# Kernel optimization log

Hardware: AMD Instinct MI355X
Metric: run time of the kernel (lower is better)

## Reference

```python
import jax, jax.numpy as jnp
import numpy as np

LN_EPS = 1e-6
L2_EPS = 1e-12


def _l2_normalize(v):
    # tf.nn.l2_normalize: v * rsqrt(max(sum(v^2), eps))
    ss = jnp.sum(v * v, axis=-1, keepdims=True)
    return v * jax.lax.rsqrt(jnp.maximum(ss, L2_EPS))


def setup_inputs() -> dict:
    key = jax.random.key(0)
    k1, k2, k3 = jax.random.split(key, 3)
    B, S, D, V = 4, 2048, 1024, 16384
    x = jax.random.normal(k1, (B, S, D), dtype=jnp.float32)
    dict_w = jax.random.normal(k2, (V, D), dtype=jnp.float32) * (2.0 / (V + D)) ** 0.5  # glorot_normal
    ln_gamma = jnp.ones((D,), dtype=jnp.float32)
    ln_beta = jnp.zeros((D,), dtype=jnp.float32)
    o_w = jax.random.normal(k3, (D, D), dtype=jnp.float32) * (2.0 / (D + D)) ** 0.5
    return {"x": x, "dict_w": dict_w, "ln_gamma": ln_gamma, "ln_beta": ln_beta, "o_w": o_w}


def reference(x, dict_w, ln_gamma, ln_beta, o_w):
    # cosine-sim codebook lookup
    q = _l2_normalize(x)                      # [B,S,D]
    k = _l2_normalize(dict_w)                 # [V,D]
    sim = jnp.einsum('bsd,vd->bsv', q, k)     # [B,S,V]
    word_idx = jnp.argmax(sim, axis=-1)       # [B,S] int
    word_sim = jnp.max(sim, axis=-1)          # [B,S]
    z = dict_w[word_idx]                      # gather codebook rows [B,S,D]
    # straight-through estimator
    e = jax.lax.stop_gradient(z - x) + x
    # layernorm (eps=1e-6)
    mu = jnp.mean(e, axis=-1, keepdims=True)
    var = jnp.mean(jnp.square(e - mu), axis=-1, keepdims=True)
    e_ln = (e - mu) * jax.lax.rsqrt(var + LN_EPS) * ln_gamma + ln_beta
    # output projection (no bias)
    out = jnp.einsum('bsd,de->bse', e_ln, o_w)
    return word_idx, word_sim, out
```

## Files before the change

kernel.cpp:

```cpp
#include <hip/hip_runtime.h>
#include <math.h>

#define D 1024
#define V 16384
#define NROWS 8192
#define NCAND 256
#define DELTA 0.15f

typedef __bf16 bf16_t;
typedef bf16_t bf16x8 __attribute__((ext_vector_type(8)));
typedef float f32x4 __attribute__((ext_vector_type(4)));
typedef int i32x4 __attribute__((ext_vector_type(4)));

__device__ __forceinline__ unsigned int sortable_key(float v) {
    unsigned int b = __float_as_uint(v);
    return (b & 0x80000000u) ? ~b : (b | 0x80000000u);
}
__device__ __forceinline__ float unkey(unsigned int key) {
    unsigned int b = (key & 0x80000000u) ? (key & 0x7FFFFFFFu) : ~key;
    return __uint_as_float(b);
}
__device__ __forceinline__ void split4(float4 v, uint2& hw, uint2& lw) {
    unsigned int u0 = __float_as_uint(v.x), u1 = __float_as_uint(v.y);
    unsigned int u2 = __float_as_uint(v.z), u3 = __float_as_uint(v.w);
    float l0 = v.x - __uint_as_float(u0 & 0xFFFF0000u);
    float l1 = v.y - __uint_as_float(u1 & 0xFFFF0000u);
    float l2 = v.z - __uint_as_float(u2 & 0xFFFF0000u);
    float l3 = v.w - __uint_as_float(u3 & 0xFFFF0000u);
    hw.x = (u0 >> 16) | (u1 & 0xFFFF0000u);
    hw.y = (u2 >> 16) | (u3 & 0xFFFF0000u);
    lw.x = (__float_as_uint(l0) >> 16) | (__float_as_uint(l1) & 0xFFFF0000u);
    lw.y = (__float_as_uint(l2) >> 16) | (__float_as_uint(l3) & 0xFFFF0000u);
}

__global__ __launch_bounds__(256) void prep_kernel(const float* __restrict__ W,
                                                   const float* __restrict__ X,
                                                   float* __restrict__ RK,
                                                   float* __restrict__ RQ,
                                                   float* __restrict__ SA,
                                                   float* __restrict__ SB,
                                                   float* __restrict__ RKS,
                                                   unsigned long long* __restrict__ packed,
                                                   unsigned int* __restrict__ count) {
    int tid = threadIdx.x;
    int row = blockIdx.x * 4 + (tid >> 6);
    int lane = tid & 63;
    const float* src = (row < V) ? (W + (size_t)row * D) : (X + (size_t)(row - V) * D);
    const float4* p = (const float4*)src;
    float ss = 0.f, am = 0.f;
#pragma unroll
    for (int i = 0; i < 4; ++i) {
        float4 v = p[lane + 64 * i];
        ss += v.x * v.x + v.y * v.y + v.z * v.z + v.w * v.w;
        am = fmaxf(am, fmaxf(fmaxf(fabsf(v.x), fabsf(v.y)), fmaxf(fabsf(v.z), fabsf(v.w))));
    }
#pragma unroll
    for (int m = 32; m >= 1; m >>= 1) {
        ss += __shfl_xor(ss, m, 64);
        am = fmaxf(am, __shfl_xor(am, m, 64));
    }
    if (lane == 0) {
        float rk = rsqrtf(fmaxf(ss, 1e-12f));
        float s = am * (1.f / 127.f);
        if (row < V) {
            RK[row] = rk;
            SB[row] = s;
            RKS[row] = rk * s;
        } else {
            RQ[row - V] = rk;
            SA[row - V] = s;
            packed[row - V] = 0ull;
            count[row - V] = 0u;
        }
    }
}

__global__ __launch_bounds__(256) void pack_i8_kernel(const float* __restrict__ src,
                                                      const float* __restrict__ S,
                                                      unsigned char* __restrict__ dst) {
    int tid = threadIdx.x;
    int row = blockIdx.x;
    int k0 = tid * 4;
    float4 v = *((const float4*)(src + (size_t)row * D) + tid);
    float s = S[row];
    float inv = (s > 0.f) ? (1.f / s) : 0.f;
    int q0 = (int)rintf(v.x * inv), q1 = (int)rintf(v.y * inv);
    int q2 = (int)rintf(v.z * inv), q3 = (int)rintf(v.w * inv);
    q0 = q0 > 127 ? 127 : (q0 < -127 ? -127 : q0);
    q1 = q1 > 127 ? 127 : (q1 < -127 ? -127 : q1);
    q2 = q2 > 127 ? 127 : (q2 < -127 ? -127 : q2);
    q3 = q3 > 127 ? 127 : (q3 < -127 ? -127 : q3);
    unsigned int word = (unsigned int)(q0 & 0xFF) | ((unsigned int)(q1 & 0xFF) << 8) |
                        ((unsigned int)(q2 & 0xFF) << 16) | ((unsigned int)(q3 & 0xFF) << 24);
    int kc = k0 >> 6, kk = k0 & 63;
    int lane = (row & 15) | ((kk >> 4) << 4);
    int j0 = kk & 15;
    size_t idx = ((size_t)(row >> 4) * 16 + kc) * 1024 + lane * 16 + j0;
    *(unsigned int*)(dst + idx) = word;
}

__global__ __launch_bounds__(256, 3) void gemm1_kernel(const unsigned char* __restrict__ Xq,
                                                       const unsigned char* __restrict__ Wq,
                                                       const float* __restrict__ SA,
                                                       const float* __restrict__ RKS,
                                                       unsigned long long* __restrict__ packed,
                                                       unsigned int* __restrict__ count,
                                                       ushort* __restrict__ candCol,
                                                       int colBase, int perX) {
    __shared__ unsigned long long red[128][2];
    __shared__ float gthr[128];

    const int tid = threadIdx.x;
    const int l = tid & 63;
    const int wave = tid >> 6;
    const int wy = wave >> 1, wx = wave & 1;
    const int lin = blockIdx.x;
    const int x = lin & 7;
    const int j = lin >> 3;
    const int rt = j / perX;
    const int ctl = x * perX + (j - rt * perX);
    const int rowBase = rt * 128;
    const int cwLocal = ctl * 128;

    i32x4 acc[4][4];
#pragma unroll
    for (int mt = 0; mt < 4; ++mt)
#pragma unroll
        for (int nt = 0; nt < 4; ++nt) acc[mt][nt] = (i32x4)0;

    const unsigned char* Ab = Xq + (size_t)(rt * 8 + wy * 4) * 16384 + l * 16;
    const unsigned char* Bb = Wq + (size_t)(colBase / 16 + ctl * 8 + wx * 4) * 16384 + l * 16;

    i32x4 a0[4], b0[4], a1[4], b1[4];
#pragma unroll
    for (int t = 0; t < 4; ++t) {
        a0[t] = *(const i32x4*)(Ab + t * 16384);
        b0[t] = *(const i32x4*)(Bb + t * 16384);
    }

    for (int kc = 0; kc < 16; kc += 2) {
        if (kc + 1 < 16) {
#pragma unroll
            for (int t = 0; t < 4; ++t) {
                a1[t] = *(const i32x4*)(Ab + t * 16384 + (kc + 1) * 1024);
                b1[t] = *(const i32x4*)(Bb + t * 16384 + (kc + 1) * 1024);
            }
        }
#pragma unroll
        for (int nt = 0; nt < 4; ++nt)
#pragma unroll
            for (int mt = 0; mt < 4; ++mt)
                acc[mt][nt] = __builtin_amdgcn_mfma_i32_16x16x64_i8(a0[mt], b0[nt], acc[mt][nt], 0, 0, 0);
        if (kc + 2 < 16) {
#pragma unroll
            for (int t = 0; t < 4; ++t) {
                a0[t] = *(const i32x4*)(Ab + t * 16384 + (kc + 2) * 1024);
                b0[t] = *(const i32x4*)(Bb + t * 16384 + (kc + 2) * 1024);
            }
        }
#pragma unroll
        for (int nt = 0; nt < 4; ++nt)
#pragma unroll
            for (int mt = 0; mt < 4; ++mt)
                acc[mt][nt] = __builtin_amdgcn_mfma_i32_16x16x64_i8(a1[mt], b1[nt], acc[mt][nt], 0, 0, 0);
    }

    const int q = l >> 4, c = l & 15;
    float rk_l[4];
#pragma unroll
    for (int nt = 0; nt < 4; ++nt) rk_l[nt] = RKS[colBase + cwLocal + wx * 64 + nt * 16 + c];
#pragma unroll
    for (int mt = 0; mt < 4; ++mt) {
#pragma unroll
        for (int r = 0; r < 4; ++r) {
            float sa = SA[rowBase + wy * 64 + mt * 16 + q * 4 + r];
            unsigned long long pk = 0;
#pragma unroll
            for (int nt = 0; nt < 4; ++nt) {
                float v = (float)acc[mt][nt][r] * sa * rk_l[nt];
                int col = colBase + cwLocal + wx * 64 + nt * 16 + c;
                unsigned long long p = ((unsigned long long)sortable_key(v) << 32) |
                                       (unsigned long long)(~(unsigned int)col);
                if (p > pk) pk = p;
            }
#pragma unroll
            for (int m = 1; m < 16; m <<= 1) {
                unsigned long long o = __shfl_xor(pk, m, 64);
                if (o > pk) pk = o;
            }
            if (c == 0) red[wy * 64 + mt * 16 + q * 4 + r][wx] = pk;
        }
    }
    __syncthreads();
    if (tid < 128) {
        unsigned long long a = red[tid][0], bb = red[tid][1];
        if (bb > a) a = bb;
        unsigned long long old = atomicMax(packed + (rowBase + tid), a);
        unsigned long long g = (old > a) ? old : a;
        gthr[tid] = unkey((unsigned int)(g >> 32)) - DELTA;
    }
    __syncthreads();
#pragma unroll
    for (int mt = 0; mt < 4; ++mt) {
#pragma unroll
        for (int r = 0; r < 4; ++r) {
            int lrow = wy * 64 + mt * 16 + q * 4 + r;
            float thr = gthr[lrow];
            int grow = rowBase + lrow;
            float sa = SA[grow];
#pragma unroll
            for (int nt = 0; nt < 4; ++nt) {
                float v = (float)acc[mt][nt][r] * sa * rk_l[nt];
                if (v >= thr) {
                    unsigned int slot = atomicAdd(count + grow, 1u);
                    if (slot < NCAND) {
                        int col = colBase + cwLocal + wx * 64 + nt * 16 + c;
                        candCol[(size_t)grow * NCAND + slot] = (ushort)col;
                    }
                }
            }
        }
    }
}

__global__ __launch_bounds__(256) void rescore_kernel(const float* __restrict__ X,
                                                      const float* __restrict__ W,
                                                      const float* __restrict__ RK,
                                                      const float* __restrict__ RQ,
                                                      const unsigned int* __restrict__ count,
                                                      const ushort* __restrict__ candCol,
                                                      float* __restrict__ outIdx,
                                                      float* __restrict__ outSim,
                                                      int* __restrict__ idxArr,
                                                      float* __restrict__ MU,
                                                      float* __restrict__ RS) {
    int wave = threadIdx.x >> 6, l = threadIdx.x & 63;
    int row = blockIdx.x * 4 + wave;
    unsigned int n = count[row];
    if (n > NCAND) n = NCAND;
    const float4* X4 = (const float4*)X + (size_t)row * 256;
    unsigned long long best = 0;
    for (unsigned int i = 0; i < n; ++i) {
        int col = (int)candCol[(size_t)row * NCAND + i];
        const float4* W4 = (const float4*)W + (size_t)col * 256;
        float s = 0.f;
#pragma unroll
        for (int jj = 0; jj < 4; ++jj) {
            float4 a = X4[jj * 64 + l];
            float4 b = W4[jj * 64 + l];
            s += a.x * b.x + a.y * b.y + a.z * b.z + a.w * b.w;
        }
#pragma unroll
        for (int m = 32; m >= 1; m >>= 1) s += __shfl_xor(s, m, 64);
        float v = s * RK[col];
        unsigned long long pk = ((unsigned long long)sortable_key(v) << 32) |
                                (unsigned long long)(~(unsigned int)col);
        if (pk > best) best = pk;
    }
    int idx = (int)(~(unsigned int)(best & 0xFFFFFFFFull)) & 0xFFFF;
    const float4* Z4 = (const float4*)W + (size_t)idx * 256;
    float s = 0.f, s2 = 0.f;
#pragma unroll
    for (int jj = 0; jj < 4; ++jj) {
        float4 a = X4[jj * 64 + l];
        float4 z = Z4[jj * 64 + l];
        float4 e;
        e.x = (z.x - a.x) + a.x;
        e.y = (z.y - a.y) + a.y;
        e.z = (z.z - a.z) + a.z;
        e.w = (z.w - a.w) + a.w;
        s  += e.x + e.y + e.z + e.w;
        s2 += e.x * e.x + e.y * e.y + e.z * e.z + e.w * e.w;
    }
#pragma unroll
    for (int m = 32; m >= 1; m >>= 1) {
        s  += __shfl_xor(s, m, 64);
        s2 += __shfl_xor(s2, m, 64);
    }
    if (l == 0) {
        outIdx[row] = (float)idx;
        outSim[row] = unkey((unsigned int)(best >> 32)) * RQ[row];
        idxArr[row] = idx;
        float mean = s * (1.f / D);
        float var  = s2 * (1.f / D) - mean * mean;
        MU[row] = mean;
        RS[row] = rsqrtf(var + 1e-6f);
    }
}

__global__ __launch_bounds__(256, 2) void gemm2_kernel(const float* __restrict__ X,
                                                       const float* __restrict__ W,
                                                       const int* __restrict__ idxArr,
                                                       const float* __restrict__ MU,
                                                       const float* __restrict__ RS,
                                                       const float* __restrict__ gamma,
                                                       const float* __restrict__ beta,
                                                       const float* __restrict__ B,
                                                       float* __restrict__ Out) {
    __shared__ ushort Ah[2][8][64][8];
    __shared__ ushort Al[2][8][64][8];
    __shared__ ushort Bh2[2][8][64][8];
    __shared__ ushort Bl2[2][8][64][8];
    __shared__ float Gs[1024];
    __shared__ float Bt[1024];

    const int tid = threadIdx.x;
    const int l = tid & 63;
    const int wave = tid >> 6;
    const int wy = wave >> 1, wx = wave & 1;
    const int rowBase = blockIdx.y * 128;
    const int nBase   = blockIdx.x * 128;

    *(float4*)&Gs[tid * 4] = *(const float4*)(gamma + tid * 4);
    *(float4*)&Bt[tid * 4] = *(const float4*)(beta + tid * 4);

    f32x4 acc[4][4];
#pragma unroll
    for (int mt = 0; mt < 4; ++mt)
#pragma unroll
        for (int nt = 0; nt < 4; ++nt) acc[mt][nt] = (f32x4)0.f;

    const int srow = tid >> 3, skq = tid & 7;
    const int sn = tid & 127, sdq = tid >> 7;
    int aidx[4];
    float amu[4], ars[4];
#pragma unroll
    for (int i = 0; i < 4; ++i) {
        int grow = rowBase + srow + i * 32;
        aidx[i] = idxArr[grow];
        amu[i] = MU[grow];
        ars[i] = RS[grow];
    }

    __syncthreads();

    float4 pz[4], pxv[4], pbv[4];
#pragma unroll
    for (int i = 0; i < 4; ++i) {
        int col = skq * 4;
        pz[i]  = *(const float4*)(W + (size_t)aidx[i] * D + col);
        pxv[i] = *(const float4*)(X + (size_t)(rowBase + srow + i * 32) * D + col);
    }
#pragma unroll
    for (int i = 0; i < 4; ++i) {
        const float* bp = B + (size_t)((sdq + i * 2) * 4) * D + nBase + sn;
        pbv[i] = {bp[0], bp[D], bp[2 * D], bp[3 * D]};
    }

    for (int kc = 0; kc < 32; ++kc) {
        const int bsel = kc & 1;
#pragma unroll
        for (int i = 0; i < 4; ++i) {
            int row = srow + i * 32;
            int col = kc * 32 + skq * 4;
            float4 z = pz[i], xv = pxv[i];
            float4 g  = *(const float4*)&Gs[col];
            float4 bb = *(const float4*)&Bt[col];
            float4 a;
            a.x = (((z.x - xv.x) + xv.x) - amu[i]) * ars[i] * g.x + bb.x;
            a.y = (((z.y - xv.y) + xv.y) - amu[i]) * ars[i] * g.y + bb.y;
            a.z = (((z.z - xv.z) + xv.z) - amu[i]) * ars[i] * g.z + bb.z;
            a.w = (((z.w - xv.w) + xv.w) - amu[i]) * ars[i] * g.w + bb.w;
            uint2 hw, lw;
            split4(a, hw, lw);
            int tile = row >> 4;
            int lf = (row & 15) | ((skq >> 1) << 4);
            int j0 = (skq & 1) * 4;
            *(uint2*)&Ah[bsel][tile][lf][j0] = hw;
            *(uint2*)&Al[bsel][tile][lf][j0] = lw;
        }
#pragma unroll
        for (int i = 0; i < 4; ++i) {
            int dq = sdq + i * 2;
            uint2 hw, lw;
            split4(pbv[i], hw, lw);
            int tile = sn >> 4;
            int lf = (sn & 15) | ((dq >> 1) << 4);
            int j0 = (dq & 1) * 4;
            *(uint2*)&Bh2[bsel][tile][lf][j0] = hw;
            *(uint2*)&Bl2[bsel][tile][lf][j0] = lw;
        }
        __syncthreads();
        float4 pzn[4], pxvn[4], pbvn[4];
        if (kc < 31) {
#pragma unroll
            for (int i = 0; i < 4; ++i) {
                int col = (kc + 1) * 32 + skq * 4;
                pzn[i]  = *(const float4*)(W + (size_t)aidx[i] * D + col);
                pxvn[i] = *(const float4*)(X + (size_t)(rowBase + srow + i * 32) * D + col);
            }
#pragma unroll
            for (int i = 0; i < 4; ++i) {
                const float* bp = B + (size_t)((kc + 1) * 32 + (sdq + i * 2) * 4) * D + nBase + sn;
                pbvn[i] = {bp[0], bp[D], bp[2 * D], bp[3 * D]};
            }
        }
        bf16x8 fah[4], fal[4];
#pragma unroll
        for (int mt = 0; mt < 4; ++mt) {
            fah[mt] = *(const bf16x8*)&Ah[bsel][wy * 4 + mt][l][0];
            fal[mt] = *(const bf16x8*)&Al[bsel][wy * 4 + mt][l][0];
        }
#pragma unroll
        for (int nt = 0; nt < 4; ++nt) {
            bf16x8 bh = *(const bf16x8*)&Bh2[bsel][wx * 4 + nt][l][0];
            bf16x8 bl = *(const bf16x8*)&Bl2[bsel][wx * 4 + nt][l][0];
#pragma unroll
            for (int mt = 0; mt < 4; ++mt) {
                acc[mt][nt] = __builtin_amdgcn_mfma_f32_16x16x32_bf16(fah[mt], bh, acc[mt][nt], 0, 0, 0);
                acc[mt][nt] = __builtin_amdgcn_mfma_f32_16x16x32_bf16(fah[mt], bl, acc[mt][nt], 0, 0, 0);
                acc[mt][nt] = __builtin_amdgcn_mfma_f32_16x16x32_bf16(fal[mt], bh, acc[mt][nt], 0, 0, 0);
            }
        }
        if (kc < 31) {
#pragma unroll
            for (int i = 0; i < 4; ++i) {
                pz[i] = pzn[i]; pxv[i] = pxvn[i]; pbv[i] = pbvn[i];
            }
        }
    }

    const int q = l >> 4, c = l & 15;
#pragma unroll
    for (int mt = 0; mt < 4; ++mt)
#pragma unroll
        for (int nt = 0; nt < 4; ++nt)
#pragma unroll
            for (int r = 0; r < 4; ++r) {
                int grow = rowBase + wy * 64 + mt * 16 + q * 4 + r;
                int gcol = nBase + wx * 64 + nt * 16 + c;
                Out[(size_t)grow * D + gcol] = acc[mt][nt][r];
            }
}

extern "C" void kernel_launch(void* const* d_in, const int* in_sizes, int n_in,
                              void* d_out, int out_size, void* d_ws, size_t ws_size,
                              hipStream_t stream) {
    const float* X     = (const float*)d_in[0];
    const float* W     = (const float*)d_in[1];
    const float* gamma = (const float*)d_in[2];
    const float* beta  = (const float*)d_in[3];
    const float* OW    = (const float*)d_in[4];

    float* out    = (float*)d_out;
    float* outIdx = out;
    float* outSim = out + NROWS;
    float* outO   = out + 2 * NROWS;

    unsigned char* Xq8 = (unsigned char*)outO;
    unsigned char* Wq8 = Xq8 + (size_t)NROWS * D;
    ushort* candCol = (ushort*)(Wq8 + (size_t)V * D);
    unsigned int* count = (unsigned int*)(candCol + (size_t)NROWS * NCAND);
    float* SA  = (float*)(count + NROWS);
    float* SB  = SA + NROWS;
    float* RKS = SB + V;

    unsigned long long* packed = (unsigned long long*)d_ws;
    float* RK     = (float*)(packed + NROWS);
    float* RQ     = RK + V;
    float* MU     = RQ + NROWS;
    float* RS     = MU + NROWS;
    int*   idxArr = (int*)(RS + NROWS);

    hipLaunchKernelGGL(prep_kernel, dim3((V + NROWS) / 4), dim3(256), 0, stream,
                       W, X, RK, RQ, SA, SB, RKS, packed, count);
    hipLaunchKernelGGL(pack_i8_kernel, dim3(NROWS), dim3(256), 0, stream, X, SA, Xq8);
    hipLaunchKernelGGL(pack_i8_kernel, dim3(V), dim3(256), 0, stream, W, SB, Wq8);

    for (int ch = 0; ch < 2; ++ch) {
        int colBase = ch * 8192;
        int perX = (8192 / 128) / 8;
        hipLaunchKernelGGL(gemm1_kernel, dim3((NROWS / 128) * (8192 / 128)), dim3(256), 0, stream,
                           Xq8, Wq8, SA, RKS, packed, count, candCol, colBase, perX);
    }

    hipLaunchKernelGGL(rescore_kernel, dim3(NROWS / 4), dim3(256), 0, stream,
                       X, W, RK, RQ, count, candCol, outIdx, outSim, idxArr, MU, RS);
    hipLaunchKernelGGL(gemm2_kernel, dim3(D / 128, NROWS / 128), dim3(256), 0, stream,
                       X, W, idxArr, MU, RS, gamma, beta, OW, outO);
}
```

Measured before the change: 583.9 us.

## Stage int8 GEMM tiles through LDS with direct global-to-LDS loads

The int8 similarity GEMM used to load A and B fragments straight from global memory into registers with double buffering, so each wave fetched its own tiles and neighbouring waves loaded the same data twice. It now has all four waves copy a shared 16 KB tile per k-step into LDS using global_load_lds, then read fragments from LDS. This removes the duplicate global traffic, and the lower register use lets the launch bound target four blocks per CU instead of three. In exchange it adds two block barriers per k-step and drops the register prefetch, so loads no longer overlap with MFMA work inside a block.

Result: faster. 537.5 us (-8.0%).

```diff
diff --git a/kernel.cpp b/kernel.cpp
--- a/kernel.cpp
+++ b/kernel.cpp
@@ -31,6 +31,12 @@
     hw.y = (u2 >> 16) | (u3 & 0xFFFF0000u);
     lw.x = (__float_as_uint(l0) >> 16) | (__float_as_uint(l1) & 0xFFFF0000u);
     lw.y = (__float_as_uint(l2) >> 16) | (__float_as_uint(l3) & 0xFFFF0000u);
+}
+
+__device__ __forceinline__ void gload16(const unsigned char* g, unsigned char* s) {
+    __builtin_amdgcn_global_load_lds((const __attribute__((address_space(1))) void*)g,
+                                     (__attribute__((address_space(3))) void*)s,
+                                     16, 0, 0);
 }
 
 __global__ __launch_bounds__(256) void prep_kernel(const float* __restrict__ W,
@@ -99,7 +105,7 @@
     *(unsigned int*)(dst + idx) = word;
 }
 
-__global__ __launch_bounds__(256, 3) void gemm1_kernel(const unsigned char* __restrict__ Xq,
+__global__ __launch_bounds__(256, 4) void gemm1_kernel(const unsigned char* __restrict__ Xq,
                                                        const unsigned char* __restrict__ Wq,
                                                        const float* __restrict__ SA,
                                                        const float* __restrict__ RKS,
@@ -107,13 +113,14 @@
                                                        unsigned int* __restrict__ count,
                                                        ushort* __restrict__ candCol,
                                                        int colBase, int perX) {
+    __shared__ __align__(16) unsigned char lds[16384];
     __shared__ unsigned long long red[128][2];
     __shared__ float gthr[128];
 
     const int tid = threadIdx.x;
     const int l = tid & 63;
-    const int wave = tid >> 6;
-    const int wy = wave >> 1, wx = wave & 1;
+    const int w = tid >> 6;
+    const int wy = w >> 1, wx = w & 1;
     const int lin = blockIdx.x;
     const int x = lin & 7;
     const int j = lin >> 3;
@@ -128,41 +135,31 @@
 #pragma unroll
         for (int nt = 0; nt < 4; ++nt) acc[mt][nt] = (i32x4)0;
 
-    const unsigned char* Ab = Xq + (size_t)(rt * 8 + wy * 4) * 16384 + l * 16;
-    const unsigned char* Bb = Wq + (size_t)(colBase / 16 + ctl * 8 + wx * 4) * 16384 + l * 16;
-
-    i32x4 a0[4], b0[4], a1[4], b1[4];
-#pragma unroll
-    for (int t = 0; t < 4; ++t) {
-        a0[t] = *(const i32x4*)(Ab + t * 16384);
-        b0[t] = *(const i32x4*)(Bb + t * 16384);
-    }
-
-    for (int kc = 0; kc < 16; kc += 2) {
-        if (kc + 1 < 16) {
-#pragma unroll
-            for (int t = 0; t < 4; ++t) {
-                a1[t] = *(const i32x4*)(Ab + t * 16384 + (kc + 1) * 1024);
-                b1[t] = *(const i32x4*)(Bb + t * 16384 + (kc + 1) * 1024);
-            }
-        }
+    const unsigned char* As = Xq + ((size_t)(rt * 8) * 16) * 1024;
+    const unsigned char* Bs = Wq + ((size_t)((colBase >> 4) + ctl * 8) * 16) * 1024;
+
+#pragma unroll 1
+    for (int kc = 0; kc < 16; ++kc) {
+#pragma unroll
+        for (int i = 0; i < 2; ++i) {
+            int u = 2 * w + i;
+            gload16(As + ((size_t)(u * 16 + kc)) * 1024 + l * 16, lds + u * 1024);
+            gload16(Bs + ((size_t)(u * 16 + kc)) * 1024 + l * 16, lds + 8192 + u * 1024);
+        }
+        __syncthreads();
+        i32x4 af[4], bf[4];
+#pragma unroll
+        for (int mi = 0; mi < 4; ++mi)
+            af[mi] = *(const i32x4*)(lds + (wy * 4 + mi) * 1024 + l * 16);
 #pragma unroll
         for (int nt = 0; nt < 4; ++nt)
-#pragma unroll
-            for (int mt = 0; mt < 4; ++mt)
-                acc[mt][nt] = __builtin_amdgcn_mfma_i32_16x16x64_i8(a0[mt], b0[nt], acc[mt][nt], 0, 0, 0);
-        if (kc + 2 < 16) {
-#pragma unroll
-            for (int t = 0; t < 4; ++t) {
-                a0[t] = *(const i32x4*)(Ab + t * 16384 + (kc + 2) * 1024);
-                b0[t] = *(const i32x4*)(Bb + t * 16384 + (kc + 2) * 1024);
-            }
-        }
+            bf[nt] = *(const i32x4*)(lds + 8192 + (wx * 4 + nt) * 1024 + l * 16);
 #pragma unroll
         for (int nt = 0; nt < 4; ++nt)
 #pragma unroll
-            for (int mt = 0; mt < 4; ++mt)
-                acc[mt][nt] = __builtin_amdgcn_mfma_i32_16x16x64_i8(a1[mt], b1[nt], acc[mt][nt], 0, 0, 0);
+            for (int mi = 0; mi < 4; ++mi)
+                acc[mi][nt] = __builtin_amdgcn_mfma_i32_16x16x64_i8(af[mi], bf[nt], acc[mi][nt], 0, 0, 0);
+        __syncthreads();
     }
 
     const int q = l >> 4, c = l & 15;
```
